# Kernel optimization log

Hardware: AMD Instinct MI355X
Metric: run time of the kernel (lower is better)

The kernel has to match this reference:

```python
import jax, jax.numpy as jnp
import numpy as np

def setup_inputs() -> dict:
    key = jax.random.key(0)
    k1, k2, k3, k4 = jax.random.split(key, 4)
    B, T, C, D = 4, 4096, 1024, 128
    x = jax.random.normal(k1, (B, T, C), dtype=jnp.float32)
    Wq = jax.random.normal(k2, (C, D), dtype=jnp.float32) * (C ** -0.5)
    Wk = jax.random.normal(k3, (C, D), dtype=jnp.float32) * (C ** -0.5)
    Wv = jax.random.normal(k4, (C, D), dtype=jnp.float32) * (C ** -0.5)
    return {"x": x, "Wq": Wq, "Wk": Wk, "Wv": Wv}

def reference(x, Wq, Wk, Wv):
    # x: [B,T,C]; Wq/Wk/Wv: [C,D] (nn.Linear bias=False => x @ W)
    B, T, C = x.shape
    q = jnp.einsum('btc,cd->btd', x, Wq)  # [B,T,D]
    k = jnp.einsum('btc,cd->btd', x, Wk)
    v = jnp.einsum('btc,cd->btd', x, Wv)
    dk = q.shape[-1]
    scale = dk ** -0.5
    w = jnp.einsum('btd,bsd->bts', q, k) * scale  # [B,T,T]
    causal = jnp.tril(jnp.ones((T, T), dtype=bool))
    w = jnp.where(causal, w, -jnp.inf)
    w = jax.nn.softmax(w, axis=-1)
    # dropout p=0.0 => identity
    attention = jnp.einsum('bts,bsd->btd', w, v)  # [B,T,D]
    return attention
```

## Files before the change

kernel.cpp:

```cpp
#include <hip/hip_runtime.h>
#include <stdint.h>

typedef __bf16 bf16_t;
typedef bf16_t bf16x8 __attribute__((ext_vector_type(8)));
typedef float f32x4 __attribute__((ext_vector_type(4)));
typedef unsigned short us8 __attribute__((ext_vector_type(8)));
typedef unsigned short us4 __attribute__((ext_vector_type(4)));
typedef unsigned int u32x4 __attribute__((ext_vector_type(4)));

#define B_ 4
#define T_ 4096
#define C_ 1024
#define D_ 128

#define NCHUNK_PB 288
#define QSCALE 0.12751744f
#define M0 14.0f

__device__ __forceinline__ uint16_t f2bf(float f) {
    union { float f; uint32_t u; } v; v.f = f;
    uint32_t u = v.u;
    uint32_t r = (u + 0x7fffu + ((u >> 16) & 1u)) >> 16;
    return (uint16_t)r;
}

__device__ __forceinline__ uint16_t bfru(float f) {
    return (uint16_t)((__float_as_uint(f) + 0x8000u) >> 16);
}

__device__ __forceinline__ float bf2f(uint16_t u) {
    return __uint_as_float((uint32_t)u << 16);
}

__global__ __launch_bounds__(256) void prep_w(const float* __restrict__ Wq,
                                              const float* __restrict__ Wk,
                                              const float* __restrict__ Wv,
                                              uint16_t* __restrict__ WT) {
    int idx = blockIdx.x * 256 + threadIdx.x;
    if (idx >= 3 * D_ * C_) return;
    int w   = idx / (D_ * C_);
    int rem = idx - w * (D_ * C_);
    int n   = rem / C_;
    int k   = rem - n * C_;
    const float* W = (w == 0) ? Wq : (w == 1) ? Wk : Wv;
    WT[idx] = f2bf(W[(size_t)k * D_ + n]);
}

#define GST 72

__global__ __launch_bounds__(256) void qkv_gemm(const float* __restrict__ x,
                                                const uint16_t* __restrict__ WT,
                                                uint16_t* __restrict__ qb,
                                                uint16_t* __restrict__ kb,
                                                uint16_t* __restrict__ vT) {
    __shared__ __align__(16) uint16_t A_lds[64 * GST];
    __shared__ __align__(16) uint16_t W_lds[128 * GST];

    int tid  = threadIdx.x;
    int lane = tid & 63;
    int wave = tid >> 6;
    int quad = lane >> 4;
    int lx   = lane & 15;
    int wm   = wave >> 1, wn = wave & 1;

    int bx   = blockIdx.x;
    int wsel = bx % 3;
    int m0   = (bx / 3) * 64;
    const uint16_t* Wp = WT + (size_t)wsel * (D_ * C_);

    f32x4 acc[2][4];
    for (int mf = 0; mf < 2; mf++)
        for (int nf = 0; nf < 4; nf++)
            acc[mf][nf] = (f32x4){0.f, 0.f, 0.f, 0.f};

    int arow = tid >> 2, acb = (tid & 3) * 16;
    int wrow = tid >> 1, wcb = (tid & 1) * 32;

    for (int k0 = 0; k0 < C_; k0 += 64) {
        {
            const float* xp = x + (size_t)(m0 + arow) * C_ + k0 + acb;
            uint32_t d[8];
#pragma unroll
            for (int j = 0; j < 4; j++) {
                float4 f = *(const float4*)(xp + j * 4);
                uint32_t u0 = __float_as_uint(f.x) + 0x8000u;
                uint32_t u1 = __float_as_uint(f.y) + 0x8000u;
                uint32_t u2 = __float_as_uint(f.z) + 0x8000u;
                uint32_t u3 = __float_as_uint(f.w) + 0x8000u;
                d[2 * j]     = __builtin_amdgcn_perm(u1, u0, 0x07060302);
                d[2 * j + 1] = __builtin_amdgcn_perm(u3, u2, 0x07060302);
            }
            *(u32x4*)&A_lds[arow * GST + acb]     = (u32x4){d[0], d[1], d[2], d[3]};
            *(u32x4*)&A_lds[arow * GST + acb + 8] = (u32x4){d[4], d[5], d[6], d[7]};
        }
        {
            const uint16_t* wp = Wp + (size_t)wrow * C_ + k0 + wcb;
#pragma unroll
            for (int i = 0; i < 4; i++)
                *(us8*)&W_lds[wrow * GST + wcb + i * 8] = *(const us8*)(wp + i * 8);
        }
        __syncthreads();

#pragma unroll
        for (int kc = 0; kc < 2; kc++) {
            bf16x8 af[2];
#pragma unroll
            for (int mf = 0; mf < 2; mf++)
                af[mf] = *(const bf16x8*)&A_lds[(wm * 32 + mf * 16 + lx) * GST + kc * 32 + quad * 8];
#pragma unroll
            for (int nf = 0; nf < 4; nf++) {
                bf16x8 bf = *(const bf16x8*)&W_lds[(wn * 64 + nf * 16 + lx) * GST + kc * 32 + quad * 8];
                acc[0][nf] = __builtin_amdgcn_mfma_f32_16x16x32_bf16(af[0], bf, acc[0][nf], 0, 0, 0);
                acc[1][nf] = __builtin_amdgcn_mfma_f32_16x16x32_bf16(af[1], bf, acc[1][nf], 0, 0, 0);
            }
        }
        __syncthreads();
    }

    int mrow0 = m0 + wm * 32 + quad * 4;
    if (wsel == 2) {
#pragma unroll
        for (int mf = 0; mf < 2; mf++) {
            int mbase = mrow0 + mf * 16;
            int batch = mbase >> 12;
            int t     = mbase & 4095;
#pragma unroll
            for (int nf = 0; nf < 4; nf++) {
                int n = wn * 64 + nf * 16 + lx;
                us4 pv;
#pragma unroll
                for (int r = 0; r < 4; r++) pv[r] = bfru(acc[mf][nf][r]);
                *(us4*)&vT[(size_t)batch * D_ * T_ + (size_t)n * T_ + t] = pv;
            }
        }
    } else {
        uint16_t* dst = (wsel == 0) ? qb : kb;
        float sc = (wsel == 0) ? QSCALE : 1.0f;
#pragma unroll
        for (int mf = 0; mf < 2; mf++)
#pragma unroll
            for (int nf = 0; nf < 4; nf++) {
                int n = wn * 64 + nf * 16 + lx;
#pragma unroll
                for (int r = 0; r < 4; r++)
                    dst[(size_t)(mrow0 + mf * 16 + r) * D_ + n] = bfru(acc[mf][nf][r] * sc);
            }
    }
}

__global__ __launch_bounds__(256, 4) void attn(const uint16_t* __restrict__ qb,
                                               const uint16_t* __restrict__ kb,
                                               const uint16_t* __restrict__ vT,
                                               uint16_t* __restrict__ part,
                                               float* __restrict__ ml) {
    __shared__ __align__(16) uint16_t K_lds[64 * 128];
    __shared__ __align__(16) uint16_t V_lds[128 * 64];
    __shared__ __align__(16) uint16_t P_lds[4 * 16 * 64];

    int tid  = threadIdx.x;
    int lane = tid & 63;
    int wave = tid >> 6;
    int quad = lane >> 4;
    int lx   = lane & 15;
    int lx7  = lx & 7;

    int batch = blockIdx.x & 3;
    int L     = NCHUNK_PB - 1 - (blockIdx.x >> 2);
    int g = 0;
    while (g < 7 && 4 * (g + 1) * (g + 2) <= L) g++;
    int rem   = L - 4 * g * (g + 1);
    int jt    = 8 * g + rem / (g + 1);
    int chunk = rem - (rem / (g + 1)) * (g + 1);
    int lidx  = batch * NCHUNK_PB + L;

    int q0     = jt * 64;
    int st0    = chunk * 8;
    int ntiles = min(8, jt - st0 + 1);

    bf16x8 qf[4];
    {
        const uint16_t* qp = qb + (size_t)(batch * T_ + q0 + wave * 16 + lx) * D_ + quad * 8;
#pragma unroll
        for (int kc = 0; kc < 4; kc++) qf[kc] = *(const bf16x8*)(qp + kc * 32);
    }

    f32x4 o[8];
    for (int i = 0; i < 8; i++) o[i] = (f32x4){0.f, 0.f, 0.f, 0.f};
    float l_i[4] = {0.f, 0.f, 0.f, 0.f};

    int krow = tid >> 2, kc0 = (tid & 3) * 4;
    int vd   = tid >> 1, vc0 = (tid & 1) * 4;

    for (int it = 0; it < ntiles; it++) {
        int s0 = (st0 + it) * 64;
        {
            const uint16_t* kp = kb + (size_t)(batch * T_ + s0 + krow) * D_ + kc0 * 8;
#pragma unroll
            for (int i = 0; i < 4; i++)
                *(us8*)&K_lds[krow * 128 + (((kc0 + i) ^ (krow & 7)) * 8)] = *(const us8*)(kp + i * 8);
        }
        {
            const uint16_t* vp = vT + (size_t)batch * D_ * T_ + (size_t)vd * T_ + s0 + vc0 * 8;
#pragma unroll
            for (int i = 0; i < 4; i++)
                *(us8*)&V_lds[vd * 64 + (((vc0 + i) ^ (vd & 7)) * 8)] = *(const us8*)(vp + i * 8);
        }
        __syncthreads();

        f32x4 s[4];
        for (int nf = 0; nf < 4; nf++) s[nf] = (f32x4){0.f, 0.f, 0.f, 0.f};
#pragma unroll
        for (int kc = 0; kc < 4; kc++)
#pragma unroll
            for (int nf = 0; nf < 4; nf++) {
                bf16x8 kf = *(const bf16x8*)&K_lds[(nf * 16 + lx) * 128 + (((kc * 4 + quad) ^ lx7) * 8)];
                s[nf] = __builtin_amdgcn_mfma_f32_16x16x32_bf16(qf[kc], kf, s[nf], 0, 0, 0);
            }

        float p[4][4];
#pragma unroll
        for (int nf = 0; nf < 4; nf++)
#pragma unroll
            for (int r = 0; r < 4; r++) p[nf][r] = s[nf][r];

        if (st0 + it == jt) {
            int rowg = q0 + wave * 16 + quad * 4;
#pragma unroll
            for (int nf = 0; nf < 4; nf++) {
                int colg = s0 + nf * 16 + lx;
#pragma unroll
                for (int r = 0; r < 4; r++)
                    if (colg > rowg + r) p[nf][r] = -INFINITY;
            }
        }

#pragma unroll
        for (int nf = 0; nf < 4; nf++)
#pragma unroll
            for (int r = 0; r < 4; r++)
                p[nf][r] = exp2f(p[nf][r] - M0);
#pragma unroll
        for (int r = 0; r < 4; r++)
            l_i[r] += (p[0][r] + p[1][r]) + (p[2][r] + p[3][r]);

#pragma unroll
        for (int nf = 0; nf < 4; nf++)
#pragma unroll
            for (int r = 0; r < 4; r++) {
                uint32_t u  = __float_as_uint(p[nf][r]) + 0x8000u;
                uint32_t pu = (uint32_t)__shfl_xor((int)u, 1, 64);
                uint32_t pk = __builtin_amdgcn_perm(pu, u, 0x07060302);
                if ((lane & 1) == 0) {
                    int prow = quad * 4 + r;
                    int pchk = nf * 2 + (lx >> 3);
                    *(uint32_t*)&P_lds[wave * 1024 + prow * 64 + ((pchk ^ (prow & 7)) * 8) + lx7] = pk;
                }
            }

        bf16x8 pf[2];
        pf[0] = *(const bf16x8*)&P_lds[wave * 1024 + lx * 64 + ((quad ^ lx7) * 8)];
        pf[1] = *(const bf16x8*)&P_lds[wave * 1024 + lx * 64 + (((4 + quad) ^ lx7) * 8)];
#pragma unroll
        for (int nf = 0; nf < 8; nf++)
#pragma unroll
            for (int kc = 0; kc < 2; kc++) {
                bf16x8 vf = *(const bf16x8*)&V_lds[(nf * 16 + lx) * 64 + (((kc * 4 + quad) ^ lx7) * 8)];
                o[nf] = __builtin_amdgcn_mfma_f32_16x16x32_bf16(pf[kc], vf, o[nf], 0, 0, 0);
            }
        __syncthreads();
    }

#pragma unroll
    for (int off = 1; off < 16; off <<= 1)
#pragma unroll
        for (int r = 0; r < 4; r++)
            l_i[r] += __shfl_xor(l_i[r], off, 64);

    uint16_t* pp = part + (size_t)lidx * (64 * 128);
#pragma unroll
    for (int nf = 0; nf < 8; nf++)
#pragma unroll
        for (int r = 0; r < 4; r++) {
            int lrow = wave * 16 + quad * 4 + r;
            pp[lrow * 128 + nf * 16 + lx] = bfru(o[nf][r]);
        }
    if (lx == 0) {
#pragma unroll
        for (int r = 0; r < 4; r++)
            ml[(size_t)lidx * 64 + wave * 16 + quad * 4 + r] = l_i[r];
    }
}

__global__ __launch_bounds__(256) void combine(const uint16_t* __restrict__ part,
                                               const float* __restrict__ ml,
                                               float* __restrict__ out) {
    int bidx  = blockIdx.x;
    int batch = bidx >> 6;
    int jt    = bidx & 63;
    int g     = jt >> 3;
    int base  = batch * NCHUNK_PB + jt + g * (jt - 4 * g - 4);
    int nch   = g + 1;

    int tid  = threadIdx.x;
    int lrow = tid >> 2;
    int c0   = (tid & 3) * 32;

    float Lsum = 0.f;
    f32x4 acc[8];
#pragma unroll
    for (int i = 0; i < 8; i++) acc[i] = (f32x4){0.f, 0.f, 0.f, 0.f};

    for (int c = 0; c < nch; c++) {
        Lsum += ml[(size_t)(base + c) * 64 + lrow];
        const uint16_t* p = part + (size_t)(base + c) * (64 * 128) + lrow * 128 + c0;
#pragma unroll
        for (int i = 0; i < 4; i++) {
            us8 v = *(const us8*)(p + i * 8);
#pragma unroll
            for (int j = 0; j < 8; j++)
                acc[i * 2 + (j >> 2)][j & 3] += bf2f(v[j]);
        }
    }
    float inv = 1.f / Lsum;
    size_t row = (size_t)(batch * T_ + jt * 64 + lrow);
#pragma unroll
    for (int i = 0; i < 8; i++)
        *(f32x4*)(out + row * 128 + c0 + i * 4) = acc[i] * inv;
}

extern "C" void kernel_launch(void* const* d_in, const int* in_sizes, int n_in,
                              void* d_out, int out_size, void* d_ws, size_t ws_size,
                              hipStream_t stream) {
    const float* x  = (const float*)d_in[0];
    const float* Wq = (const float*)d_in[1];
    const float* Wk = (const float*)d_in[2];
    const float* Wv = (const float*)d_in[3];
    float* out = (float*)d_out;

    uint16_t* ws = (uint16_t*)d_ws;
    uint16_t* qb = ws;
    uint16_t* kb = qb + (size_t)16384 * 128;
    uint16_t* vT = kb + (size_t)16384 * 128;
    uint16_t* WT = vT + (size_t)16384 * 128;
    uint16_t* part = WT + (size_t)3 * D_ * C_;
    float* ml = (float*)(part + (size_t)4 * NCHUNK_PB * 64 * 128);

    prep_w<<<dim3((3 * D_ * C_ + 255) / 256), dim3(256), 0, stream>>>(Wq, Wk, Wv, WT);
    qkv_gemm<<<dim3(3 * (16384 / 64)), dim3(256), 0, stream>>>(x, WT, qb, kb, vT);
    attn<<<dim3(B_ * NCHUNK_PB), dim3(256), 0, stream>>>(qb, kb, vT, part, ml);
    combine<<<dim3(B_ * (T_ / 64)), dim3(256), 0, stream>>>(part, ml, out);
}
```

Before: 202.2 us.

## Double attention query tile to 128 rows per block to reuse K/V tiles

Each attention block now processes 128 query rows (32 per wave, two MFMA row fragments) against up to four 64-key tiles, so every K/V tile loaded into LDS feeds twice as many query rows. The chunk schedule, partial-buffer layout and the combine kernel are reworked for 128-row tiles, and waves whose rows lie entirely above a tile's diagonal skip its compute. The cost is higher register pressure (occupancy hint lowered from 4 to 3), a larger P buffer in LDS, fewer blocks, and a simpler per-element bf16 P store that drops the packed shuffle write.

Measured after the change: 229.3 us. 13.4% more time.

```diff
diff --git a/kernel.cpp b/kernel.cpp
--- a/kernel.cpp
+++ b/kernel.cpp
@@ -13,7 +13,7 @@
 #define C_ 1024
 #define D_ 128
 
-#define NCHUNK_PB 288
+#define NCHUNK_PB 272
 #define QSCALE 0.12751744f
 #define M0 14.0f
 
@@ -148,14 +148,14 @@
     }
 }
 
-__global__ __launch_bounds__(256, 4) void attn(const uint16_t* __restrict__ qb,
+__global__ __launch_bounds__(256, 3) void attn(const uint16_t* __restrict__ qb,
                                                const uint16_t* __restrict__ kb,
                                                const uint16_t* __restrict__ vT,
                                                uint16_t* __restrict__ part,
                                                float* __restrict__ ml) {
     __shared__ __align__(16) uint16_t K_lds[64 * 128];
     __shared__ __align__(16) uint16_t V_lds[128 * 64];
-    __shared__ __align__(16) uint16_t P_lds[4 * 16 * 64];
+    __shared__ __align__(16) uint16_t P_lds[4 * 32 * 64];
 
     int tid  = threadIdx.x;
     int lane = tid & 63;
@@ -166,27 +166,32 @@
 
     int batch = blockIdx.x & 3;
     int L     = NCHUNK_PB - 1 - (blockIdx.x >> 2);
-    int g = 0;
-    while (g < 7 && 4 * (g + 1) * (g + 2) <= L) g++;
-    int rem   = L - 4 * g * (g + 1);
-    int jt    = 8 * g + rem / (g + 1);
-    int chunk = rem - (rem / (g + 1)) * (g + 1);
-    int lidx  = batch * NCHUNK_PB + L;
-
-    int q0     = jt * 64;
-    int st0    = chunk * 8;
-    int ntiles = min(8, jt - st0 + 1);
-
-    bf16x8 qf[4];
-    {
-        const uint16_t* qp = qb + (size_t)(batch * T_ + q0 + wave * 16 + lx) * D_ + quad * 8;
-#pragma unroll
-        for (int kc = 0; kc < 4; kc++) qf[kc] = *(const bf16x8*)(qp + kc * 32);
-    }
-
-    f32x4 o[8];
-    for (int i = 0; i < 8; i++) o[i] = (f32x4){0.f, 0.f, 0.f, 0.f};
-    float l_i[4] = {0.f, 0.f, 0.f, 0.f};
+    int m = 0;
+    while (m < 15 && (m + 1) * (m + 2) <= L) m++;
+    int jt2, chunk;
+    if (L >= (m + 1) * (m + 1)) { jt2 = 2 * m + 1; chunk = L - (m + 1) * (m + 1); }
+    else                        { jt2 = 2 * m;     chunk = L - m * (m + 1); }
+    int lidx = batch * NCHUNK_PB + L;
+
+    int q0     = jt2 * 128;
+    int st0    = chunk * 4;
+    int ntiles = min(4, 2 * jt2 + 2 - st0);
+    int wrow0  = q0 + wave * 32;
+
+    bf16x8 qf[2][4];
+#pragma unroll
+    for (int mf = 0; mf < 2; mf++) {
+        const uint16_t* qp = qb + (size_t)(batch * T_ + wrow0 + mf * 16 + lx) * D_ + quad * 8;
+#pragma unroll
+        for (int kc = 0; kc < 4; kc++) qf[mf][kc] = *(const bf16x8*)(qp + kc * 32);
+    }
+
+    f32x4 o[2][8];
+#pragma unroll
+    for (int mf = 0; mf < 2; mf++)
+#pragma unroll
+        for (int i = 0; i < 8; i++) o[mf][i] = (f32x4){0.f, 0.f, 0.f, 0.f};
+    float l_i[2][4] = {{0.f, 0.f, 0.f, 0.f}, {0.f, 0.f, 0.f, 0.f}};
 
     int krow = tid >> 2, kc0 = (tid & 3) * 4;
     int vd   = tid >> 1, vc0 = (tid & 1) * 4;
@@ -207,87 +212,79 @@
         }
         __syncthreads();
 
-        f32x4 s[4];
-        for (int nf = 0; nf < 4; nf++) s[nf] = (f32x4){0.f, 0.f, 0.f, 0.f};
-#pragma unroll
-        for (int kc = 0; kc < 4; kc++)
-#pragma unroll
-            for (int nf = 0; nf < 4; nf++) {
-                bf16x8 kf = *(const bf16x8*)&K_lds[(nf * 16 + lx) * 128 + (((kc * 4 + quad) ^ lx7) * 8)];
-                s[nf] = __builtin_amdgcn_mfma_f32_16x16x32_bf16(qf[kc], kf, s[nf], 0, 0, 0);
-            }
-
-        float p[4][4];
-#pragma unroll
-        for (int nf = 0; nf < 4; nf++)
-#pragma unroll
-            for (int r = 0; r < 4; r++) p[nf][r] = s[nf][r];
-
-        if (st0 + it == jt) {
-            int rowg = q0 + wave * 16 + quad * 4;
-#pragma unroll
-            for (int nf = 0; nf < 4; nf++) {
-                int colg = s0 + nf * 16 + lx;
-#pragma unroll
-                for (int r = 0; r < 4; r++)
-                    if (colg > rowg + r) p[nf][r] = -INFINITY;
-            }
-        }
-
-#pragma unroll
-        for (int nf = 0; nf < 4; nf++)
+        if (s0 <= wrow0 + 31) {
+#pragma unroll
+            for (int mf = 0; mf < 2; mf++) {
+                f32x4 s[4];
+                for (int nf = 0; nf < 4; nf++) s[nf] = (f32x4){0.f, 0.f, 0.f, 0.f};
+#pragma unroll
+                for (int kc = 0; kc < 4; kc++)
+#pragma unroll
+                    for (int nf = 0; nf < 4; nf++) {
+                        bf16x8 kf = *(const bf16x8*)&K_lds[(nf * 16 + lx) * 128 + (((kc * 4 + quad) ^ lx7) * 8)];
+                        s[nf] = __builtin_amdgcn_mfma_f32_16x16x32_bf16(qf[mf][kc], kf, s[nf], 0, 0, 0);
+                    }
+
+                int  rowg     = wrow0 + mf * 16 + quad * 4;
+                bool needmask = (s0 + 63 > wrow0 + mf * 16);
+#pragma unroll
+                for (int nf = 0; nf < 4; nf++) {
+                    int colg = s0 + nf * 16 + lx;
+#pragma unroll
+                    for (int r = 0; r < 4; r++) {
+                        float sv = s[nf][r];
+                        if (needmask && (colg > rowg + r)) sv = -INFINITY;
+                        float e = exp2f(sv - M0);
+                        l_i[mf][r] += e;
+                        int prow = mf * 16 + quad * 4 + r;
+                        int c    = nf * 2 + (lx >> 3);
+                        P_lds[wave * 2048 + prow * 64 + ((c ^ (prow & 7)) * 8) + lx7] = bfru(e);
+                    }
+                }
+            }
+
+            bf16x8 pf[2][2];
+#pragma unroll
+            for (int mf = 0; mf < 2; mf++)
+#pragma unroll
+                for (int kc = 0; kc < 2; kc++)
+                    pf[mf][kc] = *(const bf16x8*)&P_lds[wave * 2048 + (mf * 16 + lx) * 64 + (((kc * 4 + quad) ^ lx7) * 8)];
+#pragma unroll
+            for (int nf2 = 0; nf2 < 8; nf2++)
+#pragma unroll
+                for (int kc = 0; kc < 2; kc++) {
+                    bf16x8 vf = *(const bf16x8*)&V_lds[(nf2 * 16 + lx) * 64 + (((kc * 4 + quad) ^ lx7) * 8)];
+                    o[0][nf2] = __builtin_amdgcn_mfma_f32_16x16x32_bf16(pf[0][kc], vf, o[0][nf2], 0, 0, 0);
+                    o[1][nf2] = __builtin_amdgcn_mfma_f32_16x16x32_bf16(pf[1][kc], vf, o[1][nf2], 0, 0, 0);
+                }
+        }
+        __syncthreads();
+    }
+
+#pragma unroll
+    for (int off = 1; off < 16; off <<= 1)
+#pragma unroll
+        for (int mf = 0; mf < 2; mf++)
 #pragma unroll
             for (int r = 0; r < 4; r++)
-                p[nf][r] = exp2f(p[nf][r] - M0);
-#pragma unroll
-        for (int r = 0; r < 4; r++)
-            l_i[r] += (p[0][r] + p[1][r]) + (p[2][r] + p[3][r]);
-
-#pragma unroll
-        for (int nf = 0; nf < 4; nf++)
+                l_i[mf][r] += __shfl_xor(l_i[mf][r], off, 64);
+
+    uint16_t* pp = part + (size_t)lidx * (128 * 128);
+#pragma unroll
+    for (int mf = 0; mf < 2; mf++)
+#pragma unroll
+        for (int nf2 = 0; nf2 < 8; nf2++)
 #pragma unroll
             for (int r = 0; r < 4; r++) {
-                uint32_t u  = __float_as_uint(p[nf][r]) + 0x8000u;
-                uint32_t pu = (uint32_t)__shfl_xor((int)u, 1, 64);
-                uint32_t pk = __builtin_amdgcn_perm(pu, u, 0x07060302);
-                if ((lane & 1) == 0) {
-                    int prow = quad * 4 + r;
-                    int pchk = nf * 2 + (lx >> 3);
-                    *(uint32_t*)&P_lds[wave * 1024 + prow * 64 + ((pchk ^ (prow & 7)) * 8) + lx7] = pk;
-                }
-            }
-
-        bf16x8 pf[2];
-        pf[0] = *(const bf16x8*)&P_lds[wave * 1024 + lx * 64 + ((quad ^ lx7) * 8)];
-        pf[1] = *(const bf16x8*)&P_lds[wave * 1024 + lx * 64 + (((4 + quad) ^ lx7) * 8)];
-#pragma unroll
-        for (int nf = 0; nf < 8; nf++)
-#pragma unroll
-            for (int kc = 0; kc < 2; kc++) {
-                bf16x8 vf = *(const bf16x8*)&V_lds[(nf * 16 + lx) * 64 + (((kc * 4 + quad) ^ lx7) * 8)];
-                o[nf] = __builtin_amdgcn_mfma_f32_16x16x32_bf16(pf[kc], vf, o[nf], 0, 0, 0);
-            }
-        __syncthreads();
-    }
-
-#pragma unroll
-    for (int off = 1; off < 16; off <<= 1)
-#pragma unroll
-        for (int r = 0; r < 4; r++)
-            l_i[r] += __shfl_xor(l_i[r], off, 64);
-
-    uint16_t* pp = part + (size_t)lidx * (64 * 128);
-#pragma unroll
-    for (int nf = 0; nf < 8; nf++)
-#pragma unroll
-        for (int r = 0; r < 4; r++) {
-            int lrow = wave * 16 + quad * 4 + r;
-            pp[lrow * 128 + nf * 16 + lx] = bfru(o[nf][r]);
-        }
+                int lrow = wave * 32 + mf * 16 + quad * 4 + r;
+                pp[lrow * 128 + nf2 * 16 + lx] = bfru(o[mf][nf2][r]);
+            }
     if (lx == 0) {
 #pragma unroll
-        for (int r = 0; r < 4; r++)
-            ml[(size_t)lidx * 64 + wave * 16 + quad * 4 + r] = l_i[r];
+        for (int mf = 0; mf < 2; mf++)
+#pragma unroll
+            for (int r = 0; r < 4; r++)
+                ml[(size_t)lidx * 128 + wave * 32 + mf * 16 + quad * 4 + r] = l_i[mf][r];
     }
 }
 
@@ -295,26 +292,26 @@
                                                const float* __restrict__ ml,
                                                float* __restrict__ out) {
     int bidx  = blockIdx.x;
-    int batch = bidx >> 6;
-    int jt    = bidx & 63;
-    int g     = jt >> 3;
-    int base  = batch * NCHUNK_PB + jt + g * (jt - 4 * g - 4);
-    int nch   = g + 1;
+    int batch = bidx >> 5;
+    int jt2   = bidx & 31;
+    int h     = jt2 >> 1;
+    int base  = batch * NCHUNK_PB + ((jt2 & 1) ? (h + 1) * (h + 1) : h * (h + 1));
+    int nch   = (jt2 + 2) >> 1;
 
     int tid  = threadIdx.x;
-    int lrow = tid >> 2;
-    int c0   = (tid & 3) * 32;
+    int lrow = tid >> 1;
+    int c0   = (tid & 1) * 64;
 
     float Lsum = 0.f;
-    f32x4 acc[8];
-#pragma unroll
-    for (int i = 0; i < 8; i++) acc[i] = (f32x4){0.f, 0.f, 0.f, 0.f};
+    f32x4 acc[16];
+#pragma unroll
+    for (int i = 0; i < 16; i++) acc[i] = (f32x4){0.f, 0.f, 0.f, 0.f};
 
     for (int c = 0; c < nch; c++) {
-        Lsum += ml[(size_t)(base + c) * 64 + lrow];
-        const uint16_t* p = part + (size_t)(base + c) * (64 * 128) + lrow * 128 + c0;
-#pragma unroll
-        for (int i = 0; i < 4; i++) {
+        Lsum += ml[(size_t)(base + c) * 128 + lrow];
+        const uint16_t* p = part + (size_t)(base + c) * (128 * 128) + lrow * 128 + c0;
+#pragma unroll
+        for (int i = 0; i < 8; i++) {
             us8 v = *(const us8*)(p + i * 8);
 #pragma unroll
             for (int j = 0; j < 8; j++)
@@ -322,9 +319,9 @@
         }
     }
     float inv = 1.f / Lsum;
-    size_t row = (size_t)(batch * T_ + jt * 64 + lrow);
-#pragma unroll
-    for (int i = 0; i < 8; i++)
+    size_t row = (size_t)(batch * T_ + jt2 * 128 + lrow);
+#pragma unroll
+    for (int i = 0; i < 16; i++)
         *(f32x4*)(out + row * 128 + c0 + i * 4) = acc[i] * inv;
 }
 
@@ -343,10 +340,10 @@
     uint16_t* vT = kb + (size_t)16384 * 128;
     uint16_t* WT = vT + (size_t)16384 * 128;
     uint16_t* part = WT + (size_t)3 * D_ * C_;
-    float* ml = (float*)(part + (size_t)4 * NCHUNK_PB * 64 * 128);
+    float* ml = (float*)(part + (size_t)4 * NCHUNK_PB * 128 * 128);
 
     prep_w<<<dim3((3 * D_ * C_ + 255) / 256), dim3(256), 0, stream>>>(Wq, Wk, Wv, WT);
     qkv_gemm<<<dim3(3 * (16384 / 64)), dim3(256), 0, stream>>>(x, WT, qb, kb, vT);
     attn<<<dim3(B_ * NCHUNK_PB), dim3(256), 0, stream>>>(qb, kb, vT, part, ml);
-    combine<<<dim3(B_ * (T_ / 64)), dim3(256), 0, stream>>>(part, ml, out);
-}
+    combine<<<dim3(B_ * (T_ / 128)), dim3(256), 0, stream>>>(part, ml, out);
+}
```
